# Performance work log

Measured on AMD Instinct MI355X. Metric: run time of the kernel, lower is better.

The kernel has to match this reference:

```python
import jax, jax.numpy as jnp
import numpy as np

GROUPS = 32
EPS = 1e-6


def group_norm(x, scale, bias):
    b, c, h, w = x.shape
    xg = x.reshape(b, GROUPS, c // GROUPS, h, w)
    mean = xg.mean(axis=(2, 3, 4), keepdims=True)
    var = xg.var(axis=(2, 3, 4), keepdims=True)
    xg = (xg - mean) * jax.lax.rsqrt(var + EPS)
    x = xg.reshape(b, c, h, w)
    return x * scale[None, :, None, None] + bias[None, :, None, None]


def conv1x1(x, w, b):
    # x: [B,C,H,W], w: [O,C], b: [O]
    return jnp.einsum('bchw,oc->bohw', x, w) + b[None, :, None, None]


def setup_inputs() -> dict:
    key = jax.random.key(0)
    ks = jax.random.split(key, 11)
    B, C, H, W = 4, 512, 64, 64
    s = 1.0 / np.sqrt(C)
    return {
        'x': jax.random.normal(ks[0], (B, C, H, W), jnp.float32),
        'gn_scale': jnp.ones((C,), jnp.float32),
        'gn_bias': jnp.zeros((C,), jnp.float32),
        'wq': jax.random.normal(ks[1], (C, C), jnp.float32) * s,
        'bq': jnp.zeros((C,), jnp.float32),
        'wk': jax.random.normal(ks[2], (C, C), jnp.float32) * s,
        'bk': jnp.zeros((C,), jnp.float32),
        'wv': jax.random.normal(ks[3], (C, C), jnp.float32) * s,
        'bv': jnp.zeros((C,), jnp.float32),
        'wp': jax.random.normal(ks[4], (C, C), jnp.float32) * s,
        'bp': jnp.zeros((C,), jnp.float32),
    }


def reference(x, gn_scale, gn_bias, wq, bq, wk, bk, wv, bv, wp, bp):
    b, c, h, w = x.shape
    h_ = group_norm(x, gn_scale, gn_bias)
    q = conv1x1(h_, wq, bq).reshape(b, c, h * w)  # [B,C,N]
    k = conv1x1(h_, wk, bk).reshape(b, c, h * w)
    v = conv1x1(h_, wv, bv).reshape(b, c, h * w)
    # scores[b,i,j] = sum_c q[b,c,i]*k[b,c,j] / sqrt(c)
    scores = jnp.einsum('bci,bcj->bij', q, k) * (c ** -0.5)
    attn = jax.nn.softmax(scores, axis=2)
    # out[b,c,i] = sum_j attn[b,i,j] * v[b,c,j]
    out = jnp.einsum('bij,bcj->bci', attn, v).reshape(b, c, h, w)
    out = conv1x1(out, wp, bp)
    return x + out
```

## Files before the change

kernel.cpp:

```cpp
#include <hip/hip_runtime.h>

#define CDIM 512
#define NDIM 4096
#define BATCH 4

using bf8v = __attribute__((ext_vector_type(8))) __bf16;
using f4v  = __attribute__((ext_vector_type(4))) float;

typedef __attribute__((address_space(1))) unsigned int gu32;
typedef __attribute__((address_space(3))) unsigned int lu32;

static __device__ __forceinline__ unsigned short f2bf(float f) {
  unsigned int u = __float_as_uint(f);
  u += 0x7fffu + ((u >> 16) & 1u);
  return (unsigned short)(u >> 16);
}

static __device__ __forceinline__ bf8v lds_read16(const unsigned short* p) {
  bf8v r;
  unsigned off = (unsigned)(unsigned long long)p;
  asm volatile("ds_read_b128 %0, %1" : "=v"(r) : "v"(off));
  return r;
}

__global__ __launch_bounds__(256) void gn_stats_kernel(
    const float* __restrict__ x, float* __restrict__ stats) {
  const int tid = threadIdx.x;
  const float4* xv = (const float4*)(x + (long)blockIdx.x * 65536);
  float s = 0.f, ss = 0.f;
  for (int i = tid; i < 16384; i += 256) {
    float4 d = xv[i];
    s  += d.x + d.y + d.z + d.w;
    ss += d.x * d.x + d.y * d.y + d.z * d.z + d.w * d.w;
  }
#pragma unroll
  for (int off = 32; off; off >>= 1) {
    s  += __shfl_down(s, off);
    ss += __shfl_down(ss, off);
  }
  __shared__ float red[8];
  if ((tid & 63) == 0) { red[tid >> 6] = s; red[4 + (tid >> 6)] = ss; }
  __syncthreads();
  if (tid == 0) {
    float S  = red[0] + red[1] + red[2] + red[3];
    float SS = red[4] + red[5] + red[6] + red[7];
    float mean = S * (1.f / 65536.f);
    float var  = SS * (1.f / 65536.f) - mean * mean;
    stats[blockIdx.x * 2]     = mean;
    stats[blockIdx.x * 2 + 1] = rsqrtf(var + 1e-6f);
  }
}

__global__ __launch_bounds__(256) void gn_transpose_kernel(
    const float* __restrict__ x, const float* __restrict__ gs,
    const float* __restrict__ gb, const float* __restrict__ stats,
    unsigned short* __restrict__ hT) {
  __shared__ float t[64][65];
  const int tid = threadIdx.x;
  const int b = blockIdx.z;
  const long bbx = (long)b * ((long)CDIM * NDIM);
  const int n0 = blockIdx.x * 64, c0 = blockIdx.y * 64;
  for (int k = 0; k < 4; ++k) {
    int it = tid + k * 256;
    int c = it >> 4, no = (it & 15) << 2;
    int ch = c0 + c;
    int g = ch >> 4;
    float mean = stats[(b * 32 + g) * 2];
    float rstd = stats[(b * 32 + g) * 2 + 1];
    float a  = rstd * gs[ch];
    float bb = gb[ch] - mean * a;
    float4 d = *(const float4*)&x[bbx + (long)ch * NDIM + n0 + no];
    t[no + 0][c] = d.x * a + bb;
    t[no + 1][c] = d.y * a + bb;
    t[no + 2][c] = d.z * a + bb;
    t[no + 3][c] = d.w * a + bb;
  }
  __syncthreads();
  const long bbh = (long)b * ((long)NDIM * CDIM);
  for (int k = 0; k < 2; ++k) {
    int it = tid + k * 256;
    int n = it >> 3, co = (it & 7) << 3;
    unsigned int ow[4];
#pragma unroll
    for (int j = 0; j < 4; ++j) {
      unsigned short lo = f2bf(t[n][co + 2 * j]);
      unsigned short hi = f2bf(t[n][co + 2 * j + 1]);
      ow[j] = (unsigned int)lo | ((unsigned int)hi << 16);
    }
    uint4 o; o.x = ow[0]; o.y = ow[1]; o.z = ow[2]; o.w = ow[3];
    *(uint4*)&hT[bbh + (long)(n0 + n) * CDIM + c0 + co] = o;
  }
}

__global__ __launch_bounds__(256) void prep_kernel(
    const float* __restrict__ wq, const float* __restrict__ wk,
    const float* __restrict__ wv, const float* __restrict__ bq,
    const float* __restrict__ bk, unsigned short* __restrict__ wqkb,
    unsigned short* __restrict__ wvb, float* __restrict__ bqk) {
  int blk = blockIdx.x;
  if (blk < 768) {
    int i = blk * 256 + threadIdx.x;
    const float* src = (blk < 256) ? wq : (blk < 512) ? wk : wv;
    unsigned short* dst = (blk < 256) ? wqkb : (blk < 512) ? (wqkb + 262144) : wvb;
    int j = i - ((blk < 256) ? 0 : (blk < 512) ? 65536 : 131072);
    float4 d = ((const float4*)src)[j];
    ushort4 o;
    o.x = f2bf(d.x); o.y = f2bf(d.y); o.z = f2bf(d.z); o.w = f2bf(d.w);
    ((ushort4*)dst)[j] = o;
  } else {
#pragma unroll
    for (int k = 0; k < 4; ++k) {
      int i = threadIdx.x + k * 256;
      bqk[i] = (i < 512) ? bq[i] : bk[i - 512];
    }
  }
}

__global__ __launch_bounds__(256) void cvt_kernel(
    const float* __restrict__ src, unsigned short* __restrict__ dst, int n4) {
  int i = blockIdx.x * 256 + threadIdx.x;
  if (i >= n4) return;
  float4 d = ((const float4*)src)[i];
  ushort4 o;
  o.x = f2bf(d.x); o.y = f2bf(d.y); o.z = f2bf(d.z); o.w = f2bf(d.w);
  ((ushort4*)dst)[i] = o;
}

template <int EPI, int ORD>
__global__ __launch_bounds__(256, 2) void gemm4(
    const unsigned short* __restrict__ A, long sA, int lA,
    const unsigned short* __restrict__ B, long sB, int lB,
    void* __restrict__ Cp, long sC,
    const float* __restrict__ bias,
    const float* __restrict__ X, long sX,
    int GX, int GY, int Nn, int K) {
  constexpr int BM = 128, BN = 128;
  constexpr int TM = 4, TN = 4;
  constexpr int LA = 4, LB = 4;

  __shared__ __align__(16) unsigned short As[2 * BM * 64];
  __shared__ __align__(16) unsigned short Bs[2 * BN * 64];

  const int tid = threadIdx.x;
  const int nwg = gridDim.x;
  const int g = (blockIdx.x & 7) * (nwg >> 3) + (blockIdx.x >> 3);
  int bx, by, bz;
  if (ORD == 0) { bx = g % GX; int t = g / GX; by = t % GY; bz = t / GY; }
  else          { by = g % GY; int t = g / GY; bx = t % GX; bz = t / GX; }

  A += (long)bz * sA;
  B += (long)bz * sB;
  const int m0 = by * BM;
  const int n0 = bx * BN;
  const int lane = tid & 63;
  const int wv = tid >> 6;
  const int wm = (wv >> 1) * 64;
  const int wn = (wv & 1) * 64;
  const int l16 = lane & 15;
  const int quad = lane >> 4;
  const int sw7 = l16 & 7;
  const int rg0 = ((0 + quad) ^ sw7) << 3;
  const int rg1 = ((4 + quad) ^ sw7) << 3;

  const int r0s  = wv * 8 + (lane >> 3);
  const int gsrc = ((lane & 7) ^ (lane >> 3)) << 3;
  const unsigned short* Ag = A + (long)(m0 + r0s) * lA + gsrc;
  const unsigned short* Bg = B + (long)(n0 + r0s) * lB + gsrc;

  const int nt = K >> 6;

  auto stage = [&](int t) {
    if (t < nt) {
      const int k0 = t << 6;
      unsigned short* Ad = As + (t & 1) * (BM * 64) + wv * 512;
      unsigned short* Bd = Bs + (t & 1) * (BN * 64) + wv * 512;
#pragma unroll
      for (int i = 0; i < LA; ++i)
        __builtin_amdgcn_global_load_lds(
            (const gu32*)(Ag + (long)i * 32 * lA + k0),
            (lu32*)(Ad + i * 2048), 16, 0, 0);
#pragma unroll
      for (int i = 0; i < LB; ++i)
        __builtin_amdgcn_global_load_lds(
            (const gu32*)(Bg + (long)i * 32 * lB + k0),
            (lu32*)(Bd + i * 2048), 16, 0, 0);
    }
  };

  f4v acc[TM][TN] = {};
  f4v accr[TM] = {};
  bf8v ones;
#pragma unroll
  for (int i = 0; i < 8; ++i) ones[i] = (__bf16)1.0f;

  bf8v bfr[TN][2];
  bf8v afA[2][2], afB[2][2];

  const unsigned short* Ab;
  const unsigned short* Bb;

  auto rdB = [&]() {
#pragma unroll
    for (int tn = 0; tn < TN; ++tn) {
      bfr[tn][0] = lds_read16(&Bb[(wn + tn * 16 + l16) * 64 + rg0]);
      bfr[tn][1] = lds_read16(&Bb[(wn + tn * 16 + l16) * 64 + rg1]);
    }
  };
  auto rdA = [&](int q, bf8v (&fr)[2][2]) {
#pragma unroll
    for (int dr = 0; dr < 2; ++dr) {
      fr[dr][0] = lds_read16(&Ab[(wm + (q * 2 + dr) * 16 + l16) * 64 + rg0]);
      fr[dr][1] = lds_read16(&Ab[(wm + (q * 2 + dr) * 16 + l16) * 64 + rg1]);
    }
  };
  auto clus = [&](int q, bf8v (&fr)[2][2]) {
    __builtin_amdgcn_s_setprio(1);
#pragma unroll
    for (int kk = 0; kk < 2; ++kk)
#pragma unroll
      for (int dr = 0; dr < 2; ++dr) {
        const int tm = q * 2 + dr;
#pragma unroll
        for (int tn = 0; tn < TN; ++tn)
          acc[tm][tn] = __builtin_amdgcn_mfma_f32_16x16x32_bf16(
              fr[dr][kk], bfr[tn][kk], acc[tm][tn], 0, 0, 0);
        if (EPI == 3)
          accr[tm] = __builtin_amdgcn_mfma_f32_16x16x32_bf16(
              fr[dr][kk], ones, accr[tm], 0, 0, 0);
      }
    __builtin_amdgcn_s_setprio(0);
  };

  stage(0);
  for (int t = 0; t < nt; ++t) {
    asm volatile("s_waitcnt vmcnt(0)");
    __builtin_amdgcn_s_barrier();
    stage(t + 1);
    Ab = As + (t & 1) * (BM * 64);
    Bb = Bs + (t & 1) * (BN * 64);
    rdB();
    rdA(0, afA);
    rdA(1, afB);
    asm volatile("s_waitcnt lgkmcnt(4)");
    __builtin_amdgcn_sched_barrier(0);
    clus(0, afA);
    asm volatile("s_waitcnt lgkmcnt(0)");
    __builtin_amdgcn_sched_barrier(0);
    clus(1, afB);
  }

  if (EPI == 2) {
#pragma unroll
    for (int tm = 0; tm < TM; ++tm) {
#pragma unroll
      for (int r = 0; r < 4; ++r) {
        const int row = m0 + wm + tm * 16 + quad * 4 + r;
#pragma unroll
        for (int tn = 0; tn < TN; ++tn) {
          const int col = n0 + wn + tn * 16 + l16;
          float e = __expf(acc[tm][tn][r] * 0.044194173824159216f);
          ((unsigned short*)Cp)[(long)bz * sC + (long)row * Nn + col] = f2bf(e);
        }
      }
    }
  } else if (EPI == 3) {
#pragma unroll
    for (int tm = 0; tm < TM; ++tm) {
#pragma unroll
      for (int r = 0; r < 4; ++r) {
        const int row = m0 + wm + tm * 16 + quad * 4 + r;
        const float inv = 1.0f / accr[tm][r];
#pragma unroll
        for (int tn = 0; tn < TN; ++tn) {
          const int col = n0 + wn + tn * 16 + l16;
          ((unsigned short*)Cp)[(long)bz * sC + (long)row * Nn + col] =
              f2bf(acc[tm][tn][r] * inv);
        }
      }
    }
  } else {
#pragma unroll
    for (int tm = 0; tm < TM; ++tm) {
#pragma unroll
      for (int tn = 0; tn < TN; ++tn) {
        const int col = n0 + wn + tn * 16 + l16;
#pragma unroll
        for (int r = 0; r < 4; ++r) {
          const int row = m0 + wm + tm * 16 + quad * 4 + r;
          float val = acc[tm][tn][r];
          if (EPI == 0) {
            val += bias[col];
            ((unsigned short*)Cp)[(long)bz * sC + (long)row * Nn + col] = f2bf(val);
          } else if (EPI == 1) {
            val += bias[row];
            ((unsigned short*)Cp)[(long)bz * sC + (long)row * Nn + col] = f2bf(val);
          } else {
            ((float*)Cp)[(long)bz * sC + (long)row * Nn + col] =
                val + bias[row] + X[(long)bz * sX + (long)row * Nn + col];
          }
        }
      }
    }
  }
}

extern "C" void kernel_launch(void* const* d_in, const int* in_sizes, int n_in,
                              void* d_out, int out_size, void* d_ws, size_t ws_size,
                              hipStream_t stream) {
  (void)in_sizes; (void)n_in; (void)out_size;
  const float* x  = (const float*)d_in[0];
  const float* gs = (const float*)d_in[1];
  const float* gb = (const float*)d_in[2];
  const float* wq = (const float*)d_in[3];
  const float* bq = (const float*)d_in[4];
  const float* wk = (const float*)d_in[5];
  const float* bk = (const float*)d_in[6];
  const float* wv = (const float*)d_in[7];
  const float* bv = (const float*)d_in[8];
  const float* wp = (const float*)d_in[9];
  const float* bp = (const float*)d_in[10];
  float* out = (float*)d_out;

  char* ws = (char*)d_ws;
  const long NC  = (long)NDIM * CDIM;
  const long NQK = (long)NDIM * 1024;
  const long BUF = NC * 2 * BATCH;
  const long NN  = (long)NDIM * NDIM;

  unsigned short* hT   = (unsigned short*)(ws);
  unsigned short* OT   = hT;
  unsigned short* qkT  = (unsigned short*)(ws + BUF);
  unsigned short* vB   = (unsigned short*)(ws + BUF * 3);
  unsigned short* sc   = (unsigned short*)(ws + BUF * 4);
  unsigned short* wqkb = sc;
  unsigned short* wvb  = (unsigned short*)(ws + BUF * 4 + 1048576);
  float* bqk           = (float*)(ws + BUF * 4 + 1572864);
  float* stats         = (float*)(ws + BUF * 4 + 1581056);
  unsigned short* wpb  = qkT;

  gn_stats_kernel<<<BATCH * 32, 256, 0, stream>>>(x, stats);
  gn_transpose_kernel<<<dim3(NDIM / 64, CDIM / 64, BATCH), 256, 0, stream>>>(x, gs, gb, stats, hT);
  prep_kernel<<<769, 256, 0, stream>>>(wq, wk, wv, bq, bk, wqkb, wvb, bqk);

  gemm4<0, 0><<<1024, 256, 0, stream>>>(
      hT, NC, CDIM, wqkb, 0, CDIM, qkT, NQK, bqk, nullptr, 0, 8, 32, 1024, CDIM);
  gemm4<1, 1><<<512, 256, 0, stream>>>(
      wvb, 0, CDIM, hT, NC, CDIM, vB, NC, bv, nullptr, 0, 32, 4, NDIM, CDIM);

  if (ws_size >= (size_t)(BUF * 4) + (size_t)(NN * 2) * BATCH) {
    gemm4<2, 0><<<4096, 256, 0, stream>>>(
        qkT, NQK, 1024, qkT + 512, NQK, 1024, sc, NN, nullptr, nullptr, 0,
        32, 32, NDIM, CDIM);
    gemm4<3, 1><<<512, 256, 0, stream>>>(
        sc, NN, NDIM, vB, NC, NDIM, OT, NC, nullptr, nullptr, 0,
        4, 32, CDIM, NDIM);
  } else {
    for (int b = 0; b < BATCH; ++b) {
      gemm4<2, 0><<<1024, 256, 0, stream>>>(
          qkT + b * NQK, 0, 1024, qkT + b * NQK + 512, 0, 1024, sc, 0,
          nullptr, nullptr, 0, 32, 32, NDIM, CDIM);
      gemm4<3, 1><<<128, 256, 0, stream>>>(
          sc, 0, NDIM, vB + b * NC, 0, NDIM, OT + b * NC, 0,
          nullptr, nullptr, 0, 4, 32, CDIM, NDIM);
    }
  }

  cvt_kernel<<<256, 256, 0, stream>>>(wp, wpb, 65536);
  gemm4<4, 1><<<512, 256, 0, stream>>>(
      wpb, 0, CDIM, OT, NC, CDIM, out, NC, bp, x, NC, 32, 4, NDIM, CDIM);
}
```

Baseline: 357.2 us.

## Stage GEMM tiles through registers instead of direct global-to-LDS loads

Replaces the global_load_lds direct-to-shared copies with register-staged global loads that are then written to swizzled LDS after the previous tile's compute. It also removes the inline-asm LDS reads and the split two-cluster MFMA schedule with partial lgkmcnt waits, leaving scheduling to the compiler with a plain __syncthreads. This adds register pressure and LDS write instructions, and may lose the hand-tuned overlap of LDS reads with MFMA.

```diff
diff --git a/kernel.cpp b/kernel.cpp
--- a/kernel.cpp
+++ b/kernel.cpp
@@ -6,21 +6,11 @@
 
 using bf8v = __attribute__((ext_vector_type(8))) __bf16;
 using f4v  = __attribute__((ext_vector_type(4))) float;
-
-typedef __attribute__((address_space(1))) unsigned int gu32;
-typedef __attribute__((address_space(3))) unsigned int lu32;
 
 static __device__ __forceinline__ unsigned short f2bf(float f) {
   unsigned int u = __float_as_uint(f);
   u += 0x7fffu + ((u >> 16) & 1u);
   return (unsigned short)(u >> 16);
-}
-
-static __device__ __forceinline__ bf8v lds_read16(const unsigned short* p) {
-  bf8v r;
-  unsigned off = (unsigned)(unsigned long long)p;
-  asm volatile("ds_read_b128 %0, %1" : "=v"(r) : "v"(off));
-  return r;
 }
 
 __global__ __launch_bounds__(256) void gn_stats_kernel(
@@ -136,7 +126,6 @@
     int GX, int GY, int Nn, int K) {
   constexpr int BM = 128, BN = 128;
   constexpr int TM = 4, TN = 4;
-  constexpr int LA = 4, LB = 4;
 
   __shared__ __align__(16) unsigned short As[2 * BM * 64];
   __shared__ __align__(16) unsigned short Bs[2 * BN * 64];
@@ -163,27 +152,31 @@
   const int rg1 = ((4 + quad) ^ sw7) << 3;
 
   const int r0s  = wv * 8 + (lane >> 3);
-  const int gsrc = ((lane & 7) ^ (lane >> 3)) << 3;
-  const unsigned short* Ag = A + (long)(m0 + r0s) * lA + gsrc;
-  const unsigned short* Bg = B + (long)(n0 + r0s) * lB + gsrc;
+  const int gcol = (lane & 7) << 3;
+  const unsigned short* Ag = A + (long)(m0 + r0s) * lA + gcol;
+  const unsigned short* Bg = B + (long)(n0 + r0s) * lB + gcol;
+  const int wrofs = r0s * 128 + ((((lane & 7) ^ (lane >> 3)) & 7) << 4);
 
   const int nt = K >> 6;
 
-  auto stage = [&](int t) {
+  uint4 rA[4], rB[4];
+  auto ldg = [&](int t) {
     if (t < nt) {
       const int k0 = t << 6;
-      unsigned short* Ad = As + (t & 1) * (BM * 64) + wv * 512;
-      unsigned short* Bd = Bs + (t & 1) * (BN * 64) + wv * 512;
-#pragma unroll
-      for (int i = 0; i < LA; ++i)
-        __builtin_amdgcn_global_load_lds(
-            (const gu32*)(Ag + (long)i * 32 * lA + k0),
-            (lu32*)(Ad + i * 2048), 16, 0, 0);
-#pragma unroll
-      for (int i = 0; i < LB; ++i)
-        __builtin_amdgcn_global_load_lds(
-            (const gu32*)(Bg + (long)i * 32 * lB + k0),
-            (lu32*)(Bd + i * 2048), 16, 0, 0);
+#pragma unroll
+      for (int i = 0; i < 4; ++i) {
+        rA[i] = *(const uint4*)(Ag + (long)i * 32 * lA + k0);
+        rB[i] = *(const uint4*)(Bg + (long)i * 32 * lB + k0);
+      }
+    }
+  };
+  auto dsw = [&](int t) {
+    char* Ad = (char*)As + (t & 1) * 16384;
+    char* Bd = (char*)Bs + (t & 1) * 16384;
+#pragma unroll
+    for (int i = 0; i < 4; ++i) {
+      *(uint4*)(Ad + i * 4096 + wrofs) = rA[i];
+      *(uint4*)(Bd + i * 4096 + wrofs) = rB[i];
     }
   };
 
@@ -193,60 +186,39 @@
 #pragma unroll
   for (int i = 0; i < 8; ++i) ones[i] = (__bf16)1.0f;
 
-  bf8v bfr[TN][2];
-  bf8v afA[2][2], afB[2][2];
-
-  const unsigned short* Ab;
-  const unsigned short* Bb;
-
-  auto rdB = [&]() {
+  ldg(0);
+  for (int t = 0; t < nt; ++t) {
+    dsw(t);
+    __syncthreads();
+    ldg(t + 1);
+    __builtin_amdgcn_sched_barrier(0);
+    const unsigned short* Ab = As + (t & 1) * (BM * 64);
+    const unsigned short* Bb = Bs + (t & 1) * (BN * 64);
+    bf8v bfr[TN][2], afr[TM][2];
 #pragma unroll
     for (int tn = 0; tn < TN; ++tn) {
-      bfr[tn][0] = lds_read16(&Bb[(wn + tn * 16 + l16) * 64 + rg0]);
-      bfr[tn][1] = lds_read16(&Bb[(wn + tn * 16 + l16) * 64 + rg1]);
-    }
-  };
-  auto rdA = [&](int q, bf8v (&fr)[2][2]) {
-#pragma unroll
-    for (int dr = 0; dr < 2; ++dr) {
-      fr[dr][0] = lds_read16(&Ab[(wm + (q * 2 + dr) * 16 + l16) * 64 + rg0]);
-      fr[dr][1] = lds_read16(&Ab[(wm + (q * 2 + dr) * 16 + l16) * 64 + rg1]);
-    }
-  };
-  auto clus = [&](int q, bf8v (&fr)[2][2]) {
+      bfr[tn][0] = *(const bf8v*)&Bb[(wn + tn * 16 + l16) * 64 + rg0];
+      bfr[tn][1] = *(const bf8v*)&Bb[(wn + tn * 16 + l16) * 64 + rg1];
+    }
+#pragma unroll
+    for (int tm = 0; tm < TM; ++tm) {
+      afr[tm][0] = *(const bf8v*)&Ab[(wm + tm * 16 + l16) * 64 + rg0];
+      afr[tm][1] = *(const bf8v*)&Ab[(wm + tm * 16 + l16) * 64 + rg1];
+    }
     __builtin_amdgcn_s_setprio(1);
 #pragma unroll
     for (int kk = 0; kk < 2; ++kk)
 #pragma unroll
-      for (int dr = 0; dr < 2; ++dr) {
-        const int tm = q * 2 + dr;
+      for (int tm = 0; tm < TM; ++tm) {
 #pragma unroll
         for (int tn = 0; tn < TN; ++tn)
           acc[tm][tn] = __builtin_amdgcn_mfma_f32_16x16x32_bf16(
-              fr[dr][kk], bfr[tn][kk], acc[tm][tn], 0, 0, 0);
+              afr[tm][kk], bfr[tn][kk], acc[tm][tn], 0, 0, 0);
         if (EPI == 3)
           accr[tm] = __builtin_amdgcn_mfma_f32_16x16x32_bf16(
-              fr[dr][kk], ones, accr[tm], 0, 0, 0);
+              afr[tm][kk], ones, accr[tm], 0, 0, 0);
       }
     __builtin_amdgcn_s_setprio(0);
-  };
-
-  stage(0);
-  for (int t = 0; t < nt; ++t) {
-    asm volatile("s_waitcnt vmcnt(0)");
-    __builtin_amdgcn_s_barrier();
-    stage(t + 1);
-    Ab = As + (t & 1) * (BM * 64);
-    Bb = Bs + (t & 1) * (BN * 64);
-    rdB();
-    rdA(0, afA);
-    rdA(1, afB);
-    asm volatile("s_waitcnt lgkmcnt(4)");
-    __builtin_amdgcn_sched_barrier(0);
-    clus(0, afA);
-    asm volatile("s_waitcnt lgkmcnt(0)");
-    __builtin_amdgcn_sched_barrier(0);
-    clus(1, afB);
   }
 
   if (EPI == 2) {
```

After: 719.0 us. 101% more time.

## Add 256x128-tile 8-wave GEMM kernel for QK projection and score GEMMs

Applied to the files above, without the earlier changes.

Introduces a new GEMM kernel with 512 threads, a 256x128 output tile and a K-step of 32, using direct global-to-LDS loads and split MFMA phases with priority hints. The QK projection and the QK^T score/exp GEMM switch to it, halving the grid. The larger tile is meant to improve operand reuse and MFMA utilisation per workgroup. It costs more registers per wave and runs twice as many barriered K iterations on smaller LDS stages.

```diff
diff --git a/kernel.cpp b/kernel.cpp
--- a/kernel.cpp
+++ b/kernel.cpp
@@ -126,6 +126,7 @@
   ((ushort4*)dst)[i] = o;
 }
 
+
 template <int EPI, int ORD>
 __global__ __launch_bounds__(256, 2) void gemm4(
     const unsigned short* __restrict__ A, long sA, int lA,
@@ -304,6 +305,166 @@
   }
 }
 
+template <int EPI, int ORD>
+__global__ __launch_bounds__(512, 4) void gemm8n(
+    const unsigned short* __restrict__ A, long sA, int lA,
+    const unsigned short* __restrict__ B, long sB, int lB,
+    void* __restrict__ Cp, long sC,
+    const float* __restrict__ bias,
+    const float* __restrict__ X, long sX,
+    int GX, int GY, int Nn, int K) {
+  constexpr int BM = 256, BN = 128;
+  constexpr int TM = 4, TN = 4;
+
+  __shared__ __align__(16) unsigned short As[2 * BM * 32];
+  __shared__ __align__(16) unsigned short Bs[2 * BN * 32];
+
+  const int tid = threadIdx.x;
+  const int nwg = gridDim.x;
+  const int g = (blockIdx.x & 7) * (nwg >> 3) + (blockIdx.x >> 3);
+  int bx, by, bz;
+  if (ORD == 0) { bx = g % GX; int t = g / GX; by = t % GY; bz = t / GY; }
+  else          { by = g % GY; int t = g / GY; bx = t % GX; bz = t / GX; }
+
+  A += (long)bz * sA;
+  B += (long)bz * sB;
+  const int m0 = by * BM;
+  const int n0 = bx * BN;
+  const int lane = tid & 63;
+  const int wv = tid >> 6;
+  const int wm = (wv >> 1) * 64;
+  const int wn = (wv & 1) * 64;
+  const int l16 = lane & 15;
+  const int quad = lane >> 4;
+  const int rg = (quad ^ ((l16 >> 1) & 3)) << 3;
+
+  const int rl = tid >> 2;
+  const int gl = tid & 3;
+  const int gsrc = (gl ^ ((rl >> 1) & 3)) << 3;
+  const unsigned short* Ag = A + (long)(m0 + rl) * lA + gsrc;
+  const unsigned short* Bg = B + (long)(n0 + rl) * lB + gsrc;
+
+  const int nt = K >> 5;
+
+  auto stage = [&](int t) {
+    if (t < nt) {
+      const int k0 = t << 5;
+      unsigned short* Ad = As + (t & 1) * (BM * 32) + wv * 512;
+      unsigned short* Bd = Bs + (t & 1) * (BN * 32) + wv * 512;
+      __builtin_amdgcn_global_load_lds((const gu32*)(Ag + k0),
+                                       (lu32*)(Ad), 16, 0, 0);
+      __builtin_amdgcn_global_load_lds((const gu32*)(Ag + (long)128 * lA + k0),
+                                       (lu32*)(Ad + 4096), 16, 0, 0);
+      __builtin_amdgcn_global_load_lds((const gu32*)(Bg + k0),
+                                       (lu32*)(Bd), 16, 0, 0);
+    }
+  };
+
+  f4v acc[TM][TN] = {};
+  f4v accr[TM] = {};
+  bf8v ones;
+#pragma unroll
+  for (int i = 0; i < 8; ++i) ones[i] = (__bf16)1.0f;
+
+  stage(0);
+  for (int t = 0; t < nt; ++t) {
+    asm volatile("s_waitcnt vmcnt(0)");
+    __builtin_amdgcn_s_barrier();
+    stage(t + 1);
+    const unsigned short* Ab = As + (t & 1) * (BM * 32);
+    const unsigned short* Bb = Bs + (t & 1) * (BN * 32);
+    bf8v af[TM], bf[TN];
+#pragma unroll
+    for (int tn = 0; tn < TN; ++tn)
+      bf[tn] = lds_read16(&Bb[(wn + tn * 16 + l16) * 32 + rg]);
+#pragma unroll
+    for (int tm = 0; tm < TM; ++tm)
+      af[tm] = lds_read16(&Ab[(wm + tm * 16 + l16) * 32 + rg]);
+    asm volatile("s_waitcnt lgkmcnt(2)");
+    __builtin_amdgcn_sched_barrier(0);
+    __builtin_amdgcn_s_setprio(1);
+#pragma unroll
+    for (int tm = 0; tm < 2; ++tm) {
+#pragma unroll
+      for (int tn = 0; tn < TN; ++tn)
+        acc[tm][tn] = __builtin_amdgcn_mfma_f32_16x16x32_bf16(
+            af[tm], bf[tn], acc[tm][tn], 0, 0, 0);
+      if (EPI == 3)
+        accr[tm] = __builtin_amdgcn_mfma_f32_16x16x32_bf16(
+            af[tm], ones, accr[tm], 0, 0, 0);
+    }
+    __builtin_amdgcn_s_setprio(0);
+    asm volatile("s_waitcnt lgkmcnt(0)");
+    __builtin_amdgcn_sched_barrier(0);
+    __builtin_amdgcn_s_setprio(1);
+#pragma unroll
+    for (int tm = 2; tm < TM; ++tm) {
+#pragma unroll
+      for (int tn = 0; tn < TN; ++tn)
+        acc[tm][tn] = __builtin_amdgcn_mfma_f32_16x16x32_bf16(
+            af[tm], bf[tn], acc[tm][tn], 0, 0, 0);
+      if (EPI == 3)
+        accr[tm] = __builtin_amdgcn_mfma_f32_16x16x32_bf16(
+            af[tm], ones, accr[tm], 0, 0, 0);
+    }
+    __builtin_amdgcn_s_setprio(0);
+  }
+
+  if (EPI == 2) {
+#pragma unroll
+    for (int tm = 0; tm < TM; ++tm) {
+#pragma unroll
+      for (int r = 0; r < 4; ++r) {
+        const int row = m0 + wm + tm * 16 + quad * 4 + r;
+#pragma unroll
+        for (int tn = 0; tn < TN; ++tn) {
+          const int col = n0 + wn + tn * 16 + l16;
+          float e = __expf(acc[tm][tn][r] * 0.044194173824159216f);
+          ((unsigned short*)Cp)[(long)bz * sC + (long)row * Nn + col] = f2bf(e);
+        }
+      }
+    }
+  } else if (EPI == 3) {
+#pragma unroll
+    for (int tm = 0; tm < TM; ++tm) {
+#pragma unroll
+      for (int r = 0; r < 4; ++r) {
+        const int row = m0 + wm + tm * 16 + quad * 4 + r;
+        const float inv = 1.0f / accr[tm][r];
+#pragma unroll
+        for (int tn = 0; tn < TN; ++tn) {
+          const int col = n0 + wn + tn * 16 + l16;
+          ((unsigned short*)Cp)[(long)bz * sC + (long)row * Nn + col] =
+              f2bf(acc[tm][tn][r] * inv);
+        }
+      }
+    }
+  } else {
+#pragma unroll
+    for (int tm = 0; tm < TM; ++tm) {
+#pragma unroll
+      for (int tn = 0; tn < TN; ++tn) {
+        const int col = n0 + wn + tn * 16 + l16;
+#pragma unroll
+        for (int r = 0; r < 4; ++r) {
+          const int row = m0 + wm + tm * 16 + quad * 4 + r;
+          float val = acc[tm][tn][r];
+          if (EPI == 0) {
+            val += bias[col];
+            ((unsigned short*)Cp)[(long)bz * sC + (long)row * Nn + col] = f2bf(val);
+          } else if (EPI == 1) {
+            val += bias[row];
+            ((unsigned short*)Cp)[(long)bz * sC + (long)row * Nn + col] = f2bf(val);
+          } else {
+            ((float*)Cp)[(long)bz * sC + (long)row * Nn + col] =
+                val + bias[row] + X[(long)bz * sX + (long)row * Nn + col];
+          }
+        }
+      }
+    }
+  }
+}
+
 extern "C" void kernel_launch(void* const* d_in, const int* in_sizes, int n_in,
                               void* d_out, int out_size, void* d_ws, size_t ws_size,
                               hipStream_t stream) {
@@ -342,23 +503,23 @@
   gn_transpose_kernel<<<dim3(NDIM / 64, CDIM / 64, BATCH), 256, 0, stream>>>(x, gs, gb, stats, hT);
   prep_kernel<<<769, 256, 0, stream>>>(wq, wk, wv, bq, bk, wqkb, wvb, bqk);
 
-  gemm4<0, 0><<<1024, 256, 0, stream>>>(
-      hT, NC, CDIM, wqkb, 0, CDIM, qkT, NQK, bqk, nullptr, 0, 8, 32, 1024, CDIM);
+  gemm8n<0, 0><<<512, 512, 0, stream>>>(
+      hT, NC, CDIM, wqkb, 0, CDIM, qkT, NQK, bqk, nullptr, 0, 8, 16, 1024, CDIM);
   gemm4<1, 1><<<512, 256, 0, stream>>>(
       wvb, 0, CDIM, hT, NC, CDIM, vB, NC, bv, nullptr, 0, 32, 4, NDIM, CDIM);
 
   if (ws_size >= (size_t)(BUF * 4) + (size_t)(NN * 2) * BATCH) {
-    gemm4<2, 0><<<4096, 256, 0, stream>>>(
+    gemm8n<2, 0><<<2048, 512, 0, stream>>>(
         qkT, NQK, 1024, qkT + 512, NQK, 1024, sc, NN, nullptr, nullptr, 0,
-        32, 32, NDIM, CDIM);
+        32, 16, NDIM, CDIM);
     gemm4<3, 1><<<512, 256, 0, stream>>>(
         sc, NN, NDIM, vB, NC, NDIM, OT, NC, nullptr, nullptr, 0,
         4, 32, CDIM, NDIM);
   } else {
     for (int b = 0; b < BATCH; ++b) {
-      gemm4<2, 0><<<1024, 256, 0, stream>>>(
+      gemm8n<2, 0><<<512, 512, 0, stream>>>(
           qkT + b * NQK, 0, 1024, qkT + b * NQK + 512, 0, 1024, sc, 0,
-          nullptr, nullptr, 0, 32, 32, NDIM, CDIM);
+          nullptr, nullptr, 0, 32, 16, NDIM, CDIM);
       gemm4<3, 1><<<128, 256, 0, stream>>>(
           sc, 0, NDIM, vB + b * NC, 0, NDIM, OT + b * NC, 0,
           nullptr, nullptr, 0, 4, 32, CDIM, NDIM);
```

After: 339.2 us. 1.05x faster.
